# Kernel optimization log

Hardware: AMD Instinct MI355X
Metric: run time of the kernel (lower is better)

## Reference

```python
import jax, jax.numpy as jnp
import numpy as np

N_NODES = 50000
N_EDGES = 800000
IN_CH = 16
HEADS = 4
OUT_CH = 128
NEG_SLOPE = 0.2  # GATv2Conv default negative_slope


def setup_inputs() -> dict:
    key = jax.random.key(0)
    k1, k2, k3, k4, k5, k6 = jax.random.split(key, 6)
    edge_feat = jax.random.normal(k1, (N_NODES, IN_CH), dtype=jnp.float32)
    edge_index = jax.random.randint(k2, (2, N_EDGES), 0, N_NODES, dtype=jnp.int64)
    s = 1.0 / np.sqrt(IN_CH)
    W_l = jax.random.normal(k3, (IN_CH, HEADS * OUT_CH), dtype=jnp.float32) * s
    W_r = jax.random.normal(k4, (IN_CH, HEADS * OUT_CH), dtype=jnp.float32) * s
    att = jax.random.normal(k5, (HEADS, OUT_CH), dtype=jnp.float32) * (1.0 / np.sqrt(OUT_CH))
    bias = jnp.zeros((HEADS * OUT_CH,), dtype=jnp.float32)
    return {"edge_feat": edge_feat, "edge_index": edge_index,
            "W_l": W_l, "W_r": W_r, "att": att, "bias": bias}


def reference(edge_feat, edge_index, W_l, W_r, att, bias):
    # GATv2Conv forward (eval mode: dropout is identity), concat=True,
    # add_self_loops=True (PyG default).
    N = edge_feat.shape[0]
    loops = jnp.arange(N, dtype=edge_index.dtype)
    ei = jnp.concatenate([edge_index, jnp.stack([loops, loops])], axis=1)
    src, dst = ei[0], ei[1]  # message flows src -> dst

    x_l = (edge_feat @ W_l).reshape(N, HEADS, OUT_CH)  # source transform
    x_r = (edge_feat @ W_r).reshape(N, HEADS, OUT_CH)  # target transform

    # edge-wise GATv2 score: a^T LeakyReLU(x_l[j] + x_r[i])
    e = jax.nn.leaky_relu(x_l[src] + x_r[dst], NEG_SLOPE)  # [E, H, C]
    score = jnp.einsum('ehc,hc->eh', e, att)               # [E, H]

    # segment softmax over incoming edges of each target node
    smax = jax.ops.segment_max(score, dst, num_segments=N)  # [N, H]
    ex = jnp.exp(score - smax[dst])
    denom = jax.ops.segment_sum(ex, dst, num_segments=N)    # [N, H]
    alpha = ex / (denom[dst] + 1e-16)                       # [E, H]

    # scatter-aggregate weighted source features
    out = jax.ops.segment_sum(alpha[:, :, None] * x_l[src], dst, num_segments=N)
    return out.reshape(N, HEADS * OUT_CH) + bias
```

## Files before the change

kernel.cpp:

```cpp
#include <hip/hip_runtime.h>
#include <math.h>

#define N_NODES 50000
#define N_EDGES 800000
#define FDIM 512
#define NEG_SLOPE 0.2f
#define CAP 64

#define GEMM_BLKS 782
#define FILL_BLKS 3125

typedef _Float16 v2h __attribute__((ext_vector_type(2)));
typedef _Float16 v8h __attribute__((ext_vector_type(8)));
typedef float f32x4 __attribute__((ext_vector_type(4)));

__device__ __forceinline__ v2h pack_h2(float a, float b) {
    v2h r; r.x = (_Float16)a; r.y = (_Float16)b; return r;
}

__global__ __launch_bounds__(256) void preproc_kernel(const float* __restrict__ feat,
                                                      const float* __restrict__ Wl,
                                                      unsigned int* __restrict__ xlb,
                                                      const int* __restrict__ ei,
                                                      int* __restrict__ deg,
                                                      int* __restrict__ bucket) {
    int t = threadIdx.x;
    if (blockIdx.x >= GEMM_BLKS) {
        bool is64 = true;
#pragma unroll
        for (int i = 0; i < 16; i++) is64 = is64 && (ei[2 * i + 1] == 0);
        int e = (blockIdx.x - GEMM_BLKS) * 256 + t;
        if (e < N_EDGES) {
            int src = is64 ? ei[2 * e] : ei[e];
            int dst = is64 ? ei[2 * (N_EDGES + e)] : ei[N_EDGES + e];
            int pos = atomicAdd(&deg[dst], 1);
            if (pos < CAP) bucket[dst * CAP + pos] = src;
        }
        return;
    }

    __shared__ float fsh[64 * 16];
    int node0 = blockIdx.x * 64;
    int nvalid = min(64, N_NODES - node0);

    float w0[16], w1[16];
#pragma unroll
    for (int k = 0; k < 16; k++) {
        float2 w = ((const float2*)(Wl + k * FDIM))[t];
        w0[k] = w.x; w1[k] = w.y;
    }
    if (t < nvalid * 4) {
        ((float4*)fsh)[t] = ((const float4*)(feat + (size_t)node0 * 16))[t];
    }
    __syncthreads();

    for (int n = 0; n < nvalid; n++) {
        const float4* fq = (const float4*)(fsh + n * 16);
        float4 q0 = fq[0], q1 = fq[1], q2 = fq[2], q3 = fq[3];
        float fr[16] = {q0.x, q0.y, q0.z, q0.w, q1.x, q1.y, q1.z, q1.w,
                        q2.x, q2.y, q2.z, q2.w, q3.x, q3.y, q3.z, q3.w};
        float a0 = 0.f, a1 = 0.f;
#pragma unroll
        for (int k = 0; k < 16; k++) {
            a0 = fmaf(fr[k], w0[k], a0);
            a1 = fmaf(fr[k], w1[k], a1);
        }
        v2h hv = pack_h2(a0, a1);
        xlb[(size_t)(node0 + n) * 256 + t] = __builtin_bit_cast(unsigned int, hv);
    }
}

#define DPP_ROR_ADD(x, ctrl) \
    ((x) + __int_as_float(__builtin_amdgcn_update_dpp(0, __float_as_int(x), (ctrl), 0xF, 0xF, true)))

__device__ __forceinline__ float score8(uint4 u, const v2h* __restrict__ xr2,
                                        const v2h* __restrict__ a2, v2h sl) {
    v2h x0 = __builtin_bit_cast(v2h, u.x);
    v2h x1 = __builtin_bit_cast(v2h, u.y);
    v2h x2 = __builtin_bit_cast(v2h, u.z);
    v2h x3 = __builtin_bit_cast(v2h, u.w);
#if __has_builtin(__builtin_amdgcn_fdot2)
    float ps = 0.f;
    v2h s;
    s = x0 + xr2[0]; s = __builtin_elementwise_max(s, s * sl);
    ps = __builtin_amdgcn_fdot2(s, a2[0], ps, false);
    s = x1 + xr2[1]; s = __builtin_elementwise_max(s, s * sl);
    ps = __builtin_amdgcn_fdot2(s, a2[1], ps, false);
    s = x2 + xr2[2]; s = __builtin_elementwise_max(s, s * sl);
    ps = __builtin_amdgcn_fdot2(s, a2[2], ps, false);
    s = x3 + xr2[3]; s = __builtin_elementwise_max(s, s * sl);
    ps = __builtin_amdgcn_fdot2(s, a2[3], ps, false);
    return ps;
#else
    v2h ps = {(_Float16)0.f, (_Float16)0.f};
    v2h s;
    s = x0 + xr2[0]; ps += __builtin_elementwise_max(s, s * sl) * a2[0];
    s = x1 + xr2[1]; ps += __builtin_elementwise_max(s, s * sl) * a2[1];
    s = x2 + xr2[2]; ps += __builtin_elementwise_max(s, s * sl) * a2[2];
    s = x3 + xr2[3]; ps += __builtin_elementwise_max(s, s * sl) * a2[3];
    return (float)ps.x + (float)ps.y;
#endif
}

__device__ __forceinline__ void load_batch(const int* __restrict__ brow, int k, int dn,
                                           int node, const char* __restrict__ xlb_b,
                                           unsigned lane16, uint4* __restrict__ u) {
    int4 q = *(const int4*)(brow + k);
    unsigned o0 = ((unsigned)((k     < dn) ? q.x : node) << 10) + lane16;
    unsigned o1 = ((unsigned)((k + 1 < dn) ? q.y : node) << 10) + lane16;
    unsigned o2 = ((unsigned)((k + 2 < dn) ? q.z : node) << 10) + lane16;
    unsigned o3 = ((unsigned)((k + 3 < dn) ? q.w : node) << 10) + lane16;
    u[0] = *(const uint4*)(xlb_b + o0);
    u[1] = *(const uint4*)(xlb_b + o1);
    u[2] = *(const uint4*)(xlb_b + o2);
    u[3] = *(const uint4*)(xlb_b + o3);
}

__device__ __forceinline__ void process_batch(const uint4* __restrict__ u, int r,
                                              const v2h* __restrict__ xr2,
                                              const v2h* __restrict__ a2, v2h sl,
                                              float* __restrict__ acc,
                                              float& m, float& d) {
    float p0 = score8(u[0], xr2, a2, sl);
    float p1 = score8(u[1], xr2, a2, sl);
    float p2 = score8(u[2], xr2, a2, sl);
    float p3 = score8(u[3], xr2, a2, sl);

    p0 = DPP_ROR_ADD(p0, 0x128); p1 = DPP_ROR_ADD(p1, 0x128);
    p2 = DPP_ROR_ADD(p2, 0x128); p3 = DPP_ROR_ADD(p3, 0x128);
    p0 = DPP_ROR_ADD(p0, 0x124); p1 = DPP_ROR_ADD(p1, 0x124);
    p2 = DPP_ROR_ADD(p2, 0x124); p3 = DPP_ROR_ADD(p3, 0x124);
    p0 = DPP_ROR_ADD(p0, 0x122); p1 = DPP_ROR_ADD(p1, 0x122);
    p2 = DPP_ROR_ADD(p2, 0x122); p3 = DPP_ROR_ADD(p3, 0x122);
    p0 = DPP_ROR_ADD(p0, 0x121); p1 = DPP_ROR_ADD(p1, 0x121);
    p2 = DPP_ROR_ADD(p2, 0x121); p3 = DPP_ROR_ADD(p3, 0x121);

    if (r < 2) p1 = -INFINITY;
    if (r < 3) p2 = -INFINITY;
    if (r < 4) p3 = -INFINITY;

    float nm = fmaxf(fmaxf(fmaxf(m, p0), fmaxf(p1, p2)), p3);
    float sc = __expf(m - nm);
    float w0 = __expf(p0 - nm);
    float w1 = __expf(p1 - nm);
    float w2 = __expf(p2 - nm);
    float w3 = __expf(p3 - nm);
    d = fmaf(d, sc, (w0 + w1) + (w2 + w3));

    v8h h0 = __builtin_bit_cast(v8h, u[0]);
    v8h h1 = __builtin_bit_cast(v8h, u[1]);
    v8h h2 = __builtin_bit_cast(v8h, u[2]);
    v8h h3 = __builtin_bit_cast(v8h, u[3]);
#pragma unroll
    for (int j = 0; j < 8; j++) {
        float v = acc[j] * sc;
        v = fmaf(w0, (float)h0[j], v);
        v = fmaf(w1, (float)h1[j], v);
        v = fmaf(w2, (float)h2[j], v);
        v = fmaf(w3, (float)h3[j], v);
        acc[j] = v;
    }
    m = nm;
}

__global__ __launch_bounds__(512) void gat_aggregate_kernel(
        const float* __restrict__ feat, const float* __restrict__ Wr,
        const float* __restrict__ att,  const float* __restrict__ bias,
        const char* __restrict__ xlb_b, const int* __restrict__ deg,
        const int* __restrict__ bucket, float* __restrict__ out) {
    int t = threadIdx.x;
    int wave = t >> 6, lane = t & 63;
    int node = blockIdx.x * 8 + wave;
    int cbase = lane * 8;
    unsigned lane16 = (unsigned)lane << 4;

    float f[16];
    {
        const float4* fp = (const float4*)(feat + (size_t)node * 16);
        float4 f0 = fp[0], f1 = fp[1], f2 = fp[2], f3 = fp[3];
        f[0]=f0.x; f[1]=f0.y; f[2]=f0.z; f[3]=f0.w;
        f[4]=f1.x; f[5]=f1.y; f[6]=f1.z; f[7]=f1.w;
        f[8]=f2.x; f[9]=f2.y; f[10]=f2.z; f[11]=f2.w;
        f[12]=f3.x; f[13]=f3.y; f[14]=f3.z; f[15]=f3.w;
    }

    float xr[8];
#pragma unroll
    for (int j = 0; j < 8; j++) xr[j] = 0.f;
#pragma unroll
    for (int k = 0; k < 16; k++) {
        float fk = f[k];
        float4 wa = *(const float4*)(Wr + k * FDIM + cbase);
        float4 wb = *(const float4*)(Wr + k * FDIM + cbase + 4);
        xr[0] = fmaf(fk, wa.x, xr[0]); xr[1] = fmaf(fk, wa.y, xr[1]);
        xr[2] = fmaf(fk, wa.z, xr[2]); xr[3] = fmaf(fk, wa.w, xr[3]);
        xr[4] = fmaf(fk, wb.x, xr[4]); xr[5] = fmaf(fk, wb.y, xr[5]);
        xr[6] = fmaf(fk, wb.z, xr[6]); xr[7] = fmaf(fk, wb.w, xr[7]);
    }
    v2h xr2[4];
    xr2[0] = pack_h2(xr[0], xr[1]);
    xr2[1] = pack_h2(xr[2], xr[3]);
    xr2[2] = pack_h2(xr[4], xr[5]);
    xr2[3] = pack_h2(xr[6], xr[7]);

    v2h a2[4];
    {
        float4 a0 = *(const float4*)(att + cbase);
        float4 a1 = *(const float4*)(att + cbase + 4);
        a2[0] = pack_h2(a0.x, a0.y);
        a2[1] = pack_h2(a0.z, a0.w);
        a2[2] = pack_h2(a1.x, a1.y);
        a2[3] = pack_h2(a1.z, a1.w);
    }
    const v2h sl = {(_Float16)NEG_SLOPE, (_Float16)NEG_SLOPE};

    float m = -INFINITY, d = 0.f;
    float acc[8];
#pragma unroll
    for (int j = 0; j < 8; j++) acc[j] = 0.f;

    int dn = min(deg[node], CAP);
    int total = dn + 1;
    const int* brow = bucket + node * CAP;

    uint4 A[4], B[4];
    load_batch(brow, 0, dn, node, xlb_b, lane16, A);
    int k = 0;
    while (true) {
        int kB = k + 4;
        bool hasB = kB < total;
        if (hasB) load_batch(brow, kB, dn, node, xlb_b, lane16, B);
        process_batch(A, total - k, xr2, a2, sl, acc, m, d);
        if (!hasB) break;
        int kA = k + 8;
        bool hasA = kA < total;
        if (hasA) load_batch(brow, kA, dn, node, xlb_b, lane16, A);
        process_batch(B, total - kB, xr2, a2, sl, acc, m, d);
        if (!hasA) break;
        k = kA;
    }

    float inv = 1.f / (d + 1e-16f);
    float4 b0 = *(const float4*)(bias + cbase);
    float4 b1 = *(const float4*)(bias + cbase + 4);
    float bb[8] = {b0.x, b0.y, b0.z, b0.w, b1.x, b1.y, b1.z, b1.w};
    float o[8];
#pragma unroll
    for (int j = 0; j < 8; j++) o[j] = fmaf(acc[j], inv, bb[j]);
    float* op = out + (size_t)node * FDIM + cbase;
    f32x4 ov0 = {o[0], o[1], o[2], o[3]};
    f32x4 ov1 = {o[4], o[5], o[6], o[7]};
    __builtin_nontemporal_store(ov0, (f32x4*)op);
    __builtin_nontemporal_store(ov1, (f32x4*)(op + 4));
}

extern "C" void kernel_launch(void* const* d_in, const int* in_sizes, int n_in,
                              void* d_out, int out_size, void* d_ws, size_t ws_size,
                              hipStream_t stream) {
    const float* feat = (const float*)d_in[0];
    const int*   ei   = (const int*)d_in[1];
    const float* Wl   = (const float*)d_in[2];
    const float* Wr   = (const float*)d_in[3];
    const float* att  = (const float*)d_in[4];
    const float* bias = (const float*)d_in[5];
    float* out = (float*)d_out;

    char* ws = (char*)d_ws;
    size_t off = 0;
    unsigned int* xlb = (unsigned int*)(ws + off); off += (size_t)N_NODES * 256 * sizeof(unsigned int);
    int* deg    = (int*)(ws + off); off += (size_t)N_NODES * sizeof(int);
    int* bucket = (int*)(ws + off); off += ((size_t)N_NODES * CAP + 16) * sizeof(int);
    (void)ws_size; (void)in_sizes; (void)n_in; (void)out_size;

    hipError_t _e = hipMemsetAsync(deg, 0, (size_t)N_NODES * sizeof(int), stream); (void)_e;
    preproc_kernel<<<GEMM_BLKS + FILL_BLKS, 256, 0, stream>>>(feat, Wl, xlb, ei, deg, bucket);
    gat_aggregate_kernel<<<N_NODES / 8, 512, 0, stream>>>(
        feat, Wr, att, bias, (const char*)xlb, deg, bucket, out);
}
```

Baseline: 322.8 us.

## Vectorize edge bucketing, pad degree counters, use exp2 and skip softmax rescale

The bucket-fill path now gives each thread 4 edges and reads them with int4 vector loads, so it needs a quarter as many blocks. Degree counters are spread to one per 64-byte line to reduce atomic contention, at the cost of a 16x larger memset. The online softmax folds log2(e) into the attention vector and uses native exp2. When no lane in the wave sees a new maximum, it skips the accumulator rescale and one exponential. The wave-wide __any check adds a branch, and the padded counters add memory traffic.

```diff
diff --git a/kernel.cpp b/kernel.cpp
--- a/kernel.cpp
+++ b/kernel.cpp
@@ -8,11 +8,19 @@
 #define CAP 64
 
 #define GEMM_BLKS 782
-#define FILL_BLKS 3125
+#define FILL_BLKS 782
+#define DEG_PAD 16
 
 typedef _Float16 v2h __attribute__((ext_vector_type(2)));
 typedef _Float16 v8h __attribute__((ext_vector_type(8)));
 typedef float f32x4 __attribute__((ext_vector_type(4)));
+
+#if __has_builtin(__builtin_amdgcn_exp2f)
+#define EXP2(x) __builtin_amdgcn_exp2f(x)
+#else
+#define EXP2(x) __expf((x) * 0.69314718056f)
+#endif
+#define LOG2E 1.44269504089f
 
 __device__ __forceinline__ v2h pack_h2(float a, float b) {
     v2h r; r.x = (_Float16)a; r.y = (_Float16)b; return r;
@@ -29,12 +37,27 @@
         bool is64 = true;
 #pragma unroll
         for (int i = 0; i < 16; i++) is64 = is64 && (ei[2 * i + 1] == 0);
-        int e = (blockIdx.x - GEMM_BLKS) * 256 + t;
-        if (e < N_EDGES) {
-            int src = is64 ? ei[2 * e] : ei[e];
-            int dst = is64 ? ei[2 * (N_EDGES + e)] : ei[N_EDGES + e];
-            int pos = atomicAdd(&deg[dst], 1);
-            if (pos < CAP) bucket[dst * CAP + pos] = src;
+        int e0 = (blockIdx.x - GEMM_BLKS) * 1024 + t * 4;
+        if (e0 < N_EDGES) {
+            int s[4], dd[4];
+            if (is64) {
+                int4 a = *(const int4*)(ei + 2 * e0);
+                int4 b = *(const int4*)(ei + 2 * e0 + 4);
+                s[0] = a.x; s[1] = a.z; s[2] = b.x; s[3] = b.z;
+                int4 c = *(const int4*)(ei + 2 * (N_EDGES + e0));
+                int4 d2 = *(const int4*)(ei + 2 * (N_EDGES + e0) + 4);
+                dd[0] = c.x; dd[1] = c.z; dd[2] = d2.x; dd[3] = d2.z;
+            } else {
+                int4 a = *(const int4*)(ei + e0);
+                s[0] = a.x; s[1] = a.y; s[2] = a.z; s[3] = a.w;
+                int4 c = *(const int4*)(ei + N_EDGES + e0);
+                dd[0] = c.x; dd[1] = c.y; dd[2] = c.z; dd[3] = c.w;
+            }
+#pragma unroll
+            for (int i = 0; i < 4; i++) {
+                int pos = atomicAdd(&deg[dd[i] << 4], 1);
+                if (pos < CAP) bucket[dd[i] * CAP + pos] = s[i];
+            }
         }
         return;
     }
@@ -139,28 +162,47 @@
     if (r < 3) p2 = -INFINITY;
     if (r < 4) p3 = -INFINITY;
 
-    float nm = fmaxf(fmaxf(fmaxf(m, p0), fmaxf(p1, p2)), p3);
-    float sc = __expf(m - nm);
-    float w0 = __expf(p0 - nm);
-    float w1 = __expf(p1 - nm);
-    float w2 = __expf(p2 - nm);
-    float w3 = __expf(p3 - nm);
-    d = fmaf(d, sc, (w0 + w1) + (w2 + w3));
+    float bm = fmaxf(fmaxf(p0, p1), fmaxf(p2, p3));
 
     v8h h0 = __builtin_bit_cast(v8h, u[0]);
     v8h h1 = __builtin_bit_cast(v8h, u[1]);
     v8h h2 = __builtin_bit_cast(v8h, u[2]);
     v8h h3 = __builtin_bit_cast(v8h, u[3]);
-#pragma unroll
-    for (int j = 0; j < 8; j++) {
-        float v = acc[j] * sc;
-        v = fmaf(w0, (float)h0[j], v);
-        v = fmaf(w1, (float)h1[j], v);
-        v = fmaf(w2, (float)h2[j], v);
-        v = fmaf(w3, (float)h3[j], v);
-        acc[j] = v;
-    }
-    m = nm;
+
+    if (__any(bm > m)) {
+        float nm = fmaxf(m, bm);
+        float sc = EXP2(m - nm);
+        float w0 = EXP2(p0 - nm);
+        float w1 = EXP2(p1 - nm);
+        float w2 = EXP2(p2 - nm);
+        float w3 = EXP2(p3 - nm);
+        d = fmaf(d, sc, (w0 + w1) + (w2 + w3));
+#pragma unroll
+        for (int j = 0; j < 8; j++) {
+            float v = acc[j] * sc;
+            v = fmaf(w0, (float)h0[j], v);
+            v = fmaf(w1, (float)h1[j], v);
+            v = fmaf(w2, (float)h2[j], v);
+            v = fmaf(w3, (float)h3[j], v);
+            acc[j] = v;
+        }
+        m = nm;
+    } else {
+        float w0 = EXP2(p0 - m);
+        float w1 = EXP2(p1 - m);
+        float w2 = EXP2(p2 - m);
+        float w3 = EXP2(p3 - m);
+        d += (w0 + w1) + (w2 + w3);
+#pragma unroll
+        for (int j = 0; j < 8; j++) {
+            float v = acc[j];
+            v = fmaf(w0, (float)h0[j], v);
+            v = fmaf(w1, (float)h1[j], v);
+            v = fmaf(w2, (float)h2[j], v);
+            v = fmaf(w3, (float)h3[j], v);
+            acc[j] = v;
+        }
+    }
 }
 
 __global__ __launch_bounds__(512) void gat_aggregate_kernel(
@@ -207,10 +249,10 @@
     {
         float4 a0 = *(const float4*)(att + cbase);
         float4 a1 = *(const float4*)(att + cbase + 4);
-        a2[0] = pack_h2(a0.x, a0.y);
-        a2[1] = pack_h2(a0.z, a0.w);
-        a2[2] = pack_h2(a1.x, a1.y);
-        a2[3] = pack_h2(a1.z, a1.w);
+        a2[0] = pack_h2(a0.x * LOG2E, a0.y * LOG2E);
+        a2[1] = pack_h2(a0.z * LOG2E, a0.w * LOG2E);
+        a2[2] = pack_h2(a1.x * LOG2E, a1.y * LOG2E);
+        a2[3] = pack_h2(a1.z * LOG2E, a1.w * LOG2E);
     }
     const v2h sl = {(_Float16)NEG_SLOPE, (_Float16)NEG_SLOPE};
 
@@ -219,7 +261,7 @@
 #pragma unroll
     for (int j = 0; j < 8; j++) acc[j] = 0.f;
 
-    int dn = min(deg[node], CAP);
+    int dn = min(deg[node << 4], CAP);
     int total = dn + 1;
     const int* brow = bucket + node * CAP;
 
@@ -268,11 +310,11 @@
     char* ws = (char*)d_ws;
     size_t off = 0;
     unsigned int* xlb = (unsigned int*)(ws + off); off += (size_t)N_NODES * 256 * sizeof(unsigned int);
-    int* deg    = (int*)(ws + off); off += (size_t)N_NODES * sizeof(int);
+    int* deg    = (int*)(ws + off); off += (size_t)N_NODES * DEG_PAD * sizeof(int);
     int* bucket = (int*)(ws + off); off += ((size_t)N_NODES * CAP + 16) * sizeof(int);
     (void)ws_size; (void)in_sizes; (void)n_in; (void)out_size;
 
-    hipError_t _e = hipMemsetAsync(deg, 0, (size_t)N_NODES * sizeof(int), stream); (void)_e;
+    hipError_t _e = hipMemsetAsync(deg, 0, (size_t)N_NODES * DEG_PAD * sizeof(int), stream); (void)_e;
     preproc_kernel<<<GEMM_BLKS + FILL_BLKS, 256, 0, stream>>>(feat, Wl, xlb, ei, deg, bucket);
     gat_aggregate_kernel<<<N_NODES / 8, 512, 0, stream>>>(
         feat, Wr, att, bias, (const char*)xlb, deg, bucket, out);
```

Result: slower. 366.6 us (+13.6%).
